# Performance work log

Measured on AMD Instinct MI355X. Metric: run time of the kernel, lower is better.

The kernel has to match this reference:

```python
import jax, jax.numpy as jnp
import numpy as np

B, C, L, F = 4096, 1000, 32, 64


def _l2norm(x, eps=1e-12):
    # torch F.normalize: x / max(||x||_2, eps)
    n = jnp.sqrt(jnp.sum(x * x, axis=-1, keepdims=True))
    return x / jnp.maximum(n, eps)


def setup_inputs() -> dict:
    key = jax.random.key(0)
    k1, k2, k3 = jax.random.split(key, 3)
    pe = jax.random.normal(k1, (B, L, F), dtype=jnp.float32)
    cm = jax.random.uniform(k2, (B,), dtype=jnp.float32)
    class_signatures = jax.random.normal(k3, (C, L, F), dtype=jnp.float32) * 0.1
    cantor_prototypes = jnp.linspace(0.0, 1.0, C, dtype=jnp.float32)
    level_resonance = jnp.ones((C, L), dtype=jnp.float32) / L
    return {
        "pe_levels": pe,
        "cantor_measures": cm,
        "class_signatures": class_signatures,
        "cantor_prototypes": cantor_prototypes,
        "level_resonance": level_resonance,
    }


def reference(pe_levels, cantor_measures, class_signatures, cantor_prototypes, level_resonance):
    eps = 1e-6
    # --- triadic compatibility ---
    pe_norm = _l2norm(pe_levels)                     # [B,L,F]
    sig_norm = _l2norm(class_signatures)             # [C,L,F]
    sims = jnp.einsum('blf,clf->bcl', pe_norm, sig_norm)
    sims = (sims + 1.0) * 0.5                        # [B,C,L]
    resonance = jax.nn.softmax(level_resonance, axis=-1)  # [C,L]
    triadic = jnp.sum(sims * resonance[None, :, :], axis=-1)  # [B,C]
    # --- self-similarity pattern (vectorized over level pairs) ---
    a = pe_levels[:, :-1, :]                         # [B,L-1,F]
    b = pe_levels[:, 1:, :]
    cos_eps = 1e-8
    dot = jnp.sum(a * b, axis=-1)
    na = jnp.maximum(jnp.sqrt(jnp.sum(a * a, axis=-1)), cos_eps)
    nb = jnp.maximum(jnp.sqrt(jnp.sum(b * b, axis=-1)), cos_eps)
    self_sim = (dot / (na * nb) + 1.0) * 0.5         # [B,L-1]
    expected = jax.nn.sigmoid(level_resonance[:, :-1] - level_resonance[:, 1:])  # [C,L-1]
    pattern_diff = jnp.abs(self_sim[:, None, :] - expected[None, :, :])  # [B,C,L-1]
    self_sim_compat = jnp.clip(1.0 - jnp.mean(pattern_diff, axis=-1), 0.0, 1.0)  # [B,C]
    # --- cantor compatibility ---
    d = jnp.abs(cantor_measures[:, None] - cantor_prototypes[None, :])
    cantor_compat = jnp.exp(-(d * d) / 0.1) + 1e-8   # [B,C]
    # --- hierarchical compatibility ---
    split = L // 2
    early = _l2norm(jnp.mean(pe_levels[:, :split, :], axis=1))          # [B,F]
    late = _l2norm(jnp.mean(pe_levels[:, split:, :], axis=1))
    early_t = _l2norm(jnp.mean(class_signatures[:, :split, :], axis=1))  # [C,F]
    late_t = _l2norm(jnp.mean(class_signatures[:, split:, :], axis=1))
    early_c = (early @ early_t.T + 1.0) * 0.5
    late_c = (late @ late_t.T + 1.0) * 0.5
    hier = (early_c + late_c) * 0.5                  # [B,C]
    # --- geometric mean of four clamped terms ---
    t = jnp.clip(triadic, eps, 1.0)
    s = jnp.clip(self_sim_compat, eps, 1.0)
    c = jnp.clip(cantor_compat, eps, 1.0)
    h = jnp.clip(hier, eps, 1.0)
    return (t * s * c * h) ** 0.25
```

## Files before the change

kernel.cpp:

```cpp
#include <hip/hip_runtime.h>
#include <hip/hip_bf16.h>

typedef float f32x4 __attribute__((ext_vector_type(4)));
typedef short bf16x8 __attribute__((ext_vector_type(8)));

#define B_DIM 4096
#define C_DIM 1000
#define CP 1024
#define K1 2048
#define EPS 1e-6f

__device__ __forceinline__ float wsum(float v) {
#pragma unroll
  for (int o = 32; o > 0; o >>= 1) v += __shfl_xor(v, o, 64);
  return v;
}
__device__ __forceinline__ float wmax(float v) {
#pragma unroll
  for (int o = 32; o > 0; o >>= 1) v = fmaxf(v, __shfl_xor(v, o, 64));
  return v;
}

__device__ __forceinline__ void load_lds16(const void* g, void* l) {
  __builtin_amdgcn_global_load_lds(
      (const __attribute__((address_space(1))) unsigned int*)g,
      (__attribute__((address_space(3))) unsigned int*)l, 16, 0, 0);
}

__global__ void prep_all(const float* __restrict__ sig,
                         const float* __restrict__ lr,
                         const float* __restrict__ pe,
                         __hip_bfloat16* __restrict__ wsig,
                         float* __restrict__ expd,
                         __hip_bfloat16* __restrict__ elc,
                         __hip_bfloat16* __restrict__ pen,
                         float* __restrict__ ssb,
                         __hip_bfloat16* __restrict__ elb) {
  __shared__ float LW[4][2304];
  __shared__ float AUX[4][32];
  const int w = threadIdx.x >> 6;
  const int t = threadIdx.x & 63;
  const int unit = blockIdx.x * 4 + w;
  const bool isClass = unit < CP;
  const int c = unit;
  const int b = unit - CP;
  const bool pad = isClass && (c >= C_DIM);
  const float* src = isClass ? (sig + (size_t)c * K1) : (pe + (size_t)b * K1);

#pragma unroll
  for (int i = 0; i < 8; ++i) {
    int o = i * 256 + t * 4;
    f32x4 v = {0.f, 0.f, 0.f, 0.f};
    if (!pad) v = *(const f32x4*)(src + o);
    *(f32x4*)&LW[w][(o >> 6) * 72 + (o & 63)] = v;
  }
  __syncthreads();

  if (isClass) {
    float lv = (t < 32 && !pad) ? lr[c * 32 + t] : -3.0e38f;
    float mx = wmax(lv);
    float ev = (t < 32 && !pad) ? expf(lv - mx) : 0.f;
    float sden = wsum(ev);
    float res = pad ? 0.f : ev / sden;
    float lvn = __shfl_down(lv, 1, 64);
    if (t < 31) {
      expd[c * 32 + t] = pad ? 0.f : 1.f / (1.f + expf(-(lv - lvn)));
    } else if (t == 31) {
      expd[c * 32 + 31] = 0.f;
    }
    if (t < 32) {
      f32x4 sq = {0.f, 0.f, 0.f, 0.f};
#pragma unroll
      for (int i = 0; i < 16; ++i) {
        f32x4 v = *(const f32x4*)&LW[w][t * 72 + i * 4];
        sq += v * v;
      }
      float s = sq[0] + sq[1] + sq[2] + sq[3];
      float inv = 1.f / fmaxf(sqrtf(s), 1e-12f);
      AUX[w][t] = inv * res;
    }
  } else {
    if (t < 32) {
      f32x4 sq = {0.f, 0.f, 0.f, 0.f}, dt = {0.f, 0.f, 0.f, 0.f};
      const int tn = (t < 31) ? t + 1 : t;
#pragma unroll
      for (int i = 0; i < 16; ++i) {
        f32x4 v = *(const f32x4*)&LW[w][t * 72 + i * 4];
        f32x4 vn = *(const f32x4*)&LW[w][tn * 72 + i * 4];
        sq += v * v;
        dt += v * vn;
      }
      float s = sq[0] + sq[1] + sq[2] + sq[3];
      float d = dt[0] + dt[1] + dt[2] + dt[3];
      float nrm = sqrtf(s);
      AUX[w][t] = 1.f / fmaxf(nrm, 1e-12f);
      float nn = __shfl_down(nrm, 1, 64);
      if (t < 31)
        ssb[(size_t)b * 32 + t] =
            (d / (fmaxf(nrm, 1e-8f) * fmaxf(nn, 1e-8f)) + 1.f) * 0.5f;
      else
        ssb[(size_t)b * 32 + 31] = 0.f;
    }
  }
  __syncthreads();

  __hip_bfloat16* dst = isClass ? (wsig + (size_t)c * K1) : (pen + (size_t)b * K1);
  float es = 0.f, ls = 0.f;
#pragma unroll
  for (int l = 0; l < 32; ++l) {
    float v = LW[w][l * 72 + t];
    float m = AUX[w][l];
    dst[l * 64 + t] = __float2bfloat16(v * m);
    if (l < 16) es += v; else ls += v;
  }
  es *= (1.f / 16.f);
  ls *= (1.f / 16.f);
  float en = fmaxf(sqrtf(wsum(es * es)), 1e-12f);
  float ln2 = fmaxf(sqrtf(wsum(ls * ls)), 1e-12f);
  __hip_bfloat16* el = isClass ? (elc + (size_t)c * 128) : (elb + (size_t)b * 128);
  el[t] = __float2bfloat16(es / en);
  el[64 + t] = __float2bfloat16(ls / ln2);
}

__global__ __launch_bounds__(512, 2)
void basin_main(const __hip_bfloat16* __restrict__ pen,
                const __hip_bfloat16* __restrict__ wsig,
                const __hip_bfloat16* __restrict__ elb,
                const __hip_bfloat16* __restrict__ elc,
                const float* __restrict__ ssb,
                const float* __restrict__ expd,
                const float* __restrict__ cm,
                const float* __restrict__ proto,
                float* __restrict__ out) {
  __shared__ __align__(16) char smem[131072];
  const int t = threadIdx.x;
  const int lane = t & 63;
  const int w = t >> 6;
  const int wm = w >> 2, wn = w & 3;
  const int brow = blockIdx.x * 128;
  const int bcol = blockIdx.y * 128;
  const int srow16 = t >> 4;
  const int sel = (((t & 15) ^ (srow16 & 15)) << 3);
  const int l15 = lane & 15;
  const int gq = lane >> 4;

  const int rowA = (wm * 64 + l15) << 8;
  const int rowB = ((wn * 32 + l15) << 8) + 32768;
  int xg[4];
#pragma unroll
  for (int kk = 0; kk < 4; ++kk) xg[kk] = (((kk * 4 + gq) ^ l15) << 4);

  f32x4 acc1[4][2] = {};
  f32x4 acc2[4][2] = {};

#define STAGE_T(kt, BI)                                                                   \
  do {                                                                                    \
    _Pragma("unroll") for (int i = 0; i < 4; ++i) {                                       \
      load_lds16(pen + (size_t)(brow + i * 32 + srow16) * K1 + (kt) * 128 + sel,          \
                 smem + (BI) * 65536 + i * 8192 + t * 16);                                \
      load_lds16(wsig + (size_t)(bcol + i * 32 + srow16) * K1 + (kt) * 128 + sel,         \
                 smem + (BI) * 65536 + 32768 + i * 8192 + t * 16);                        \
    }                                                                                     \
  } while (0)

#define STAGE_H()                                                                         \
  do {                                                                                    \
    _Pragma("unroll") for (int i = 0; i < 4; ++i) {                                       \
      load_lds16(elb + (size_t)(brow + i * 32 + srow16) * 128 + sel,                      \
                 smem + i * 8192 + t * 16);                                               \
      load_lds16(elc + (size_t)(bcol + i * 32 + srow16) * 128 + sel,                      \
                 smem + 32768 + i * 8192 + t * 16);                                       \
    }                                                                                     \
  } while (0)

#define COMPUTE(ACC, BI)                                                                  \
  do {                                                                                    \
    _Pragma("unroll") for (int kk = 0; kk < 4; ++kk) {                                    \
      bf16x8 af[4], bg[2];                                                                \
      _Pragma("unroll") for (int m = 0; m < 4; ++m)                                       \
          af[m] = *(const bf16x8*)(smem + (BI) * 65536 + rowA + m * 4096 + xg[kk]);       \
      _Pragma("unroll") for (int n = 0; n < 2; ++n)                                       \
          bg[n] = *(const bf16x8*)(smem + (BI) * 65536 + rowB + n * 4096 + xg[kk]);       \
      _Pragma("unroll") for (int m = 0; m < 4; ++m)                                       \
        _Pragma("unroll") for (int n = 0; n < 2; ++n)                                     \
          ACC[m][n] = __builtin_amdgcn_mfma_f32_16x16x32_bf16(af[m], bg[n], ACC[m][n], 0, 0, 0); \
    }                                                                                     \
  } while (0)

#define KSTEP(kt, BI, OTHER)                                                              \
  do {                                                                                    \
    asm volatile("s_waitcnt vmcnt(0)" ::: "memory");                \
    __builtin_amdgcn_s_barrier();                      \
    __builtin_amdgcn_sched_barrier(0);                                                    \
    if ((kt) + 1 < 16) STAGE_T((kt) + 1, OTHER);           \
    COMPUTE(acc1, BI);                                                                    \
  } while (0)

  STAGE_T(0, 0);
  for (int kt = 0; kt < 16; kt += 2) {
    KSTEP(kt, 0, 1);
    KSTEP(kt + 1, 1, 0);
  }
  __syncthreads();

  STAGE_H();
  asm volatile("s_waitcnt vmcnt(0)" ::: "memory");
  __builtin_amdgcn_s_barrier();
  __builtin_amdgcn_sched_barrier(0);
  COMPUTE(acc2, 0);
  __syncthreads();

  float* ss_l = (float*)smem;
  float* ex_l = (float*)(smem + 18432);
  float* cm_l = (float*)(smem + 36864);
  float* pr_l = (float*)(smem + 37376);
  for (int i = t; i < 4096; i += 512) {
    int r = i >> 5, l = i & 31;
    ss_l[r * 36 + l] = ssb[(size_t)(brow + r) * 32 + l];
    ex_l[r * 36 + l] = expd[(size_t)(bcol + r) * 32 + l];
  }
  if (t < 128) cm_l[t] = cm[brow + t];
  else if (t < 256) pr_l[t - 128] = (bcol + t - 128 < C_DIM) ? proto[bcol + t - 128] : 0.f;
  __syncthreads();

  const int col0 = wn * 32 + l15;
  const int row0 = wm * 64 + (gq << 2);
#pragma unroll
  for (int m = 0; m < 4; ++m) {
    float ssum[4][2];
#pragma unroll
    for (int j = 0; j < 4; ++j)
#pragma unroll
      for (int n = 0; n < 2; ++n) ssum[j][n] = 0.f;
#pragma unroll
    for (int l4 = 0; l4 < 32; l4 += 4) {
      f32x4 evv[2], sv[4];
#pragma unroll
      for (int n = 0; n < 2; ++n)
        evv[n] = *(const f32x4*)&ex_l[(col0 + n * 16) * 36 + l4];
#pragma unroll
      for (int j = 0; j < 4; ++j)
        sv[j] = *(const f32x4*)&ss_l[(row0 + m * 16 + j) * 36 + l4];
#pragma unroll
      for (int j = 0; j < 4; ++j)
#pragma unroll
        for (int n = 0; n < 2; ++n) {
          ssum[j][n] += fabsf(sv[j][0] - evv[n][0]) + fabsf(sv[j][1] - evv[n][1]) +
                        fabsf(sv[j][2] - evv[n][2]) + fabsf(sv[j][3] - evv[n][3]);
        }
    }
#pragma unroll
    for (int j = 0; j < 4; ++j) {
      int rloc = row0 + m * 16 + j;
      float cmv = cm_l[rloc];
#pragma unroll
      for (int n = 0; n < 2; ++n) {
        int cloc = col0 + n * 16;
        int cg = bcol + cloc;
        float tria = fminf(fmaxf(0.5f + 0.5f * acc1[m][n][j], EPS), 1.0f);
        float hier = fminf(fmaxf(0.5f + 0.25f * acc2[m][n][j], EPS), 1.0f);
        float sc = fminf(fmaxf(1.0f - ssum[j][n] * (1.0f / 31.0f), EPS), 1.0f);
        float d = cmv - pr_l[cloc];
        float cc = __expf(d * d * -10.0f) + 1e-8f;
        cc = fminf(fmaxf(cc, EPS), 1.0f);
        float p = tria * sc * cc * hier;
        if (cg < C_DIM)
          out[(size_t)(brow + rloc) * C_DIM + cg] = sqrtf(sqrtf(p));
      }
    }
  }
}

extern "C" void kernel_launch(void* const* d_in, const int* in_sizes, int n_in,
                              void* d_out, int out_size, void* d_ws, size_t ws_size,
                              hipStream_t stream) {
  (void)in_sizes; (void)n_in; (void)out_size; (void)ws_size;
  const float* pe = (const float*)d_in[0];
  const float* cm = (const float*)d_in[1];
  const float* sig = (const float*)d_in[2];
  const float* proto = (const float*)d_in[3];
  const float* lr = (const float*)d_in[4];
  float* out = (float*)d_out;
  char* ws = (char*)d_ws;

  __hip_bfloat16* wsig = (__hip_bfloat16*)(ws);
  __hip_bfloat16* pen = (__hip_bfloat16*)(ws + 4194304);
  __hip_bfloat16* elb = (__hip_bfloat16*)(ws + 20971520);
  __hip_bfloat16* elc = (__hip_bfloat16*)(ws + 22020096);
  float* ssb = (float*)(ws + 22282240);
  float* expd = (float*)(ws + 22806528);

  prep_all<<<(CP + B_DIM) / 4, 256, 0, stream>>>(sig, lr, pe, wsig, expd, elc, pen, ssb, elb);
  dim3 grid(B_DIM / 128, CP / 128);
  basin_main<<<grid, 512, 0, stream>>>(pen, wsig, elb, elc, ssb, expd, cm, proto, out);
}
```

Before: 62.40 us.

## Halve K-tile width and deepen LDS pipeline to four stages

Changes the main GEMM loop from double-buffered 128-wide K tiles to quadruple-buffered 64-wide K tiles, with three loads kept in flight and partial vmcnt waits in place of full drains. The swizzle is adjusted to an 8-way XOR for the narrower rows, and the hierarchical GEMM is split into two staged halves. The goal is to hide global-to-LDS latency behind MFMA work. In exchange the loop runs twice as many barriers, with less compute between each one, while total LDS use stays at 128 KB.

Result: faster. 59.10 us (-5.3%).

```diff
diff --git a/kernel.cpp b/kernel.cpp
--- a/kernel.cpp
+++ b/kernel.cpp
@@ -139,75 +139,87 @@
   const int wm = w >> 2, wn = w & 3;
   const int brow = blockIdx.x * 128;
   const int bcol = blockIdx.y * 128;
-  const int srow16 = t >> 4;
-  const int sel = (((t & 15) ^ (srow16 & 15)) << 3);
+  const int srow8 = t >> 3;
+  const int sel8 = (((t & 7) ^ (srow8 & 7)) << 3);
   const int l15 = lane & 15;
   const int gq = lane >> 4;
 
-  const int rowA = (wm * 64 + l15) << 8;
-  const int rowB = ((wn * 32 + l15) << 8) + 32768;
-  int xg[4];
-#pragma unroll
-  for (int kk = 0; kk < 4; ++kk) xg[kk] = (((kk * 4 + gq) ^ l15) << 4);
+  const int rowA = (wm * 64 + l15) << 7;
+  const int rowB = (wn * 32 + l15) << 7;
+  int xg[2];
+#pragma unroll
+  for (int kk = 0; kk < 2; ++kk) xg[kk] = (((kk * 4 + gq) ^ (l15 & 7)) << 4);
 
   f32x4 acc1[4][2] = {};
   f32x4 acc2[4][2] = {};
 
 #define STAGE_T(kt, BI)                                                                   \
   do {                                                                                    \
-    _Pragma("unroll") for (int i = 0; i < 4; ++i) {                                       \
-      load_lds16(pen + (size_t)(brow + i * 32 + srow16) * K1 + (kt) * 128 + sel,          \
-                 smem + (BI) * 65536 + i * 8192 + t * 16);                                \
-      load_lds16(wsig + (size_t)(bcol + i * 32 + srow16) * K1 + (kt) * 128 + sel,         \
-                 smem + (BI) * 65536 + 32768 + i * 8192 + t * 16);                        \
+    _Pragma("unroll") for (int i = 0; i < 2; ++i) {                                       \
+      load_lds16(pen + (size_t)(brow + i * 64 + srow8) * K1 + (kt) * 64 + sel8,           \
+                 smem + (BI) * 32768 + i * 8192 + t * 16);                                \
+      load_lds16(wsig + (size_t)(bcol + i * 64 + srow8) * K1 + (kt) * 64 + sel8,          \
+                 smem + (BI) * 32768 + 16384 + i * 8192 + t * 16);                        \
     }                                                                                     \
   } while (0)
 
-#define STAGE_H()                                                                         \
+#define STAGE_H(s, BI)                                                                    \
   do {                                                                                    \
-    _Pragma("unroll") for (int i = 0; i < 4; ++i) {                                       \
-      load_lds16(elb + (size_t)(brow + i * 32 + srow16) * 128 + sel,                      \
-                 smem + i * 8192 + t * 16);                                               \
-      load_lds16(elc + (size_t)(bcol + i * 32 + srow16) * 128 + sel,                      \
-                 smem + 32768 + i * 8192 + t * 16);                                       \
+    _Pragma("unroll") for (int i = 0; i < 2; ++i) {                                       \
+      load_lds16(elb + (size_t)(brow + i * 64 + srow8) * 128 + (s) * 64 + sel8,           \
+                 smem + (BI) * 32768 + i * 8192 + t * 16);                                \
+      load_lds16(elc + (size_t)(bcol + i * 64 + srow8) * 128 + (s) * 64 + sel8,           \
+                 smem + (BI) * 32768 + 16384 + i * 8192 + t * 16);                        \
     }                                                                                     \
   } while (0)
 
 #define COMPUTE(ACC, BI)                                                                  \
   do {                                                                                    \
-    _Pragma("unroll") for (int kk = 0; kk < 4; ++kk) {                                    \
+    _Pragma("unroll") for (int kk = 0; kk < 2; ++kk) {                                    \
       bf16x8 af[4], bg[2];                                                                \
       _Pragma("unroll") for (int m = 0; m < 4; ++m)                                       \
-          af[m] = *(const bf16x8*)(smem + (BI) * 65536 + rowA + m * 4096 + xg[kk]);       \
+          af[m] = *(const bf16x8*)(smem + (BI) * 32768 + rowA + m * 2048 + xg[kk]);       \
       _Pragma("unroll") for (int n = 0; n < 2; ++n)                                       \
-          bg[n] = *(const bf16x8*)(smem + (BI) * 65536 + rowB + n * 4096 + xg[kk]);       \
+          bg[n] = *(const bf16x8*)(smem + (BI) * 32768 + 16384 + rowB + n * 2048 + xg[kk]); \
       _Pragma("unroll") for (int m = 0; m < 4; ++m)                                       \
         _Pragma("unroll") for (int n = 0; n < 2; ++n)                                     \
           ACC[m][n] = __builtin_amdgcn_mfma_f32_16x16x32_bf16(af[m], bg[n], ACC[m][n], 0, 0, 0); \
     }                                                                                     \
   } while (0)
 
-#define KSTEP(kt, BI, OTHER)                                                              \
+#define VMW(N) asm volatile("s_waitcnt vmcnt(" #N ")" ::: "memory")
+#define BAR()                    \
+  __builtin_amdgcn_s_barrier();  \
+  __builtin_amdgcn_sched_barrier(0)
+
+#define KSTEP_S(kt, BI, NXT)                                                              \
   do {                                                                                    \
-    asm volatile("s_waitcnt vmcnt(0)" ::: "memory");                \
-    __builtin_amdgcn_s_barrier();                      \
-    __builtin_amdgcn_sched_barrier(0);                                                    \
-    if ((kt) + 1 < 16) STAGE_T((kt) + 1, OTHER);           \
+    VMW(8);                                                                               \
+    BAR();                                                                                \
+    STAGE_T((kt) + 3, NXT);                                                               \
     COMPUTE(acc1, BI);                                                                    \
   } while (0)
 
   STAGE_T(0, 0);
-  for (int kt = 0; kt < 16; kt += 2) {
-    KSTEP(kt, 0, 1);
-    KSTEP(kt + 1, 1, 0);
-  }
-  __syncthreads();
-
-  STAGE_H();
-  asm volatile("s_waitcnt vmcnt(0)" ::: "memory");
-  __builtin_amdgcn_s_barrier();
-  __builtin_amdgcn_sched_barrier(0);
+  STAGE_T(1, 1);
+  STAGE_T(2, 2);
+  for (int kt = 0; kt < 28; kt += 4) {
+    KSTEP_S(kt, 0, 3);
+    KSTEP_S(kt + 1, 1, 0);
+    KSTEP_S(kt + 2, 2, 1);
+    KSTEP_S(kt + 3, 3, 2);
+  }
+  VMW(8); BAR(); STAGE_T(31, 3); COMPUTE(acc1, 0);
+  VMW(8); BAR(); COMPUTE(acc1, 1);
+  VMW(4); BAR(); COMPUTE(acc1, 2);
+  VMW(0); BAR(); COMPUTE(acc1, 3);
+
+  STAGE_H(0, 0);
+  STAGE_H(1, 1);
+  VMW(4); BAR();
   COMPUTE(acc2, 0);
+  VMW(0); BAR();
+  COMPUTE(acc2, 1);
   __syncthreads();
 
   float* ss_l = (float*)smem;
```
